# Optimization experiments

Measured on AMD Instinct MI355X. Metric: run time of the kernel, lower is better.

Reference implementation:

```python
import jax, jax.numpy as jnp
import numpy as np

UNITS = 512
IN_DIM = 256


def setup_inputs() -> dict:
    key = jax.random.key(0)
    k1, k2, k3 = jax.random.split(key, 3)
    x = jax.random.normal(k1, (128, 512, IN_DIM), dtype=jnp.float32)
    # glorot_uniform for kernel
    lim = float(np.sqrt(6.0 / (IN_DIM + UNITS)))
    kernel = jax.random.uniform(k2, (IN_DIM, UNITS), minval=-lim, maxval=lim, dtype=jnp.float32)
    # orthogonal init for recurrent kernel
    a = jax.random.normal(k3, (UNITS, UNITS), dtype=jnp.float32)
    q, r = jnp.linalg.qr(a)
    recurrent_kernel = q * jnp.sign(jnp.diag(r))[None, :]
    bias = jnp.zeros((UNITS,), dtype=jnp.float32)
    return {"x": x, "kernel": kernel, "recurrent_kernel": recurrent_kernel, "bias": bias}


def reference(x, kernel, recurrent_kernel, bias):
    # h_t = tanh(x_t @ W_x + b + h_{t-1} @ W_h), return full sequence [B, T, U]
    B = x.shape[0]
    # Precompute input projection for all timesteps in one batched GEMM
    xp = jnp.einsum('btf,fu->btu', x, kernel) + bias  # [B, T, U]

    def step(h, xp_t):
        h_new = jnp.tanh(xp_t + h @ recurrent_kernel)
        return h_new, h_new

    h0 = jnp.zeros((B, UNITS), dtype=x.dtype)
    _, ys = jax.lax.scan(step, h0, jnp.swapaxes(xp, 0, 1))  # ys: [T, B, U]
    return jnp.swapaxes(ys, 0, 1)
```

## Files before the change

kernel.cpp:

```cpp
#include <hip/hip_runtime.h>
#include <math.h>


#define SENT 0xFFFFFFFFu
#define ALF(p)    __hip_atomic_load((p), __ATOMIC_RELAXED, __HIP_MEMORY_SCOPE_AGENT)
#define ASF(p, v) __hip_atomic_store((p), (v), __ATOMIC_RELAXED, __HIP_MEMORY_SCOPE_AGENT)
#define FMA4(A, W, H) { (A).x += (H)*(W).x; (A).y += (H)*(W).y; (A).z += (H)*(W).z; (A).w += (H)*(W).w; }

__global__ __launch_bounds__(256) void xp_gemm_sent(
    const float* __restrict__ x,
    const float* __restrict__ wx,
    const float* __restrict__ bias,
    float* __restrict__ xp,
    float* __restrict__ out)
{
    __shared__ float As[32][68];
    __shared__ float Bs[32][68];

    const int tid = threadIdx.x;
    const int m0 = blockIdx.y * 64;
    const int n0 = blockIdx.x * 64;
    const int tm = tid / 16;
    const int tn = tid % 16;

    {
        const float s = __uint_as_float(SENT);
        const float4 sv = make_float4(s, s, s, s);
        const int r = tid >> 4;
        const int c = (tid & 15) * 4;
        float* op = out + (size_t)m0 * 512 + n0;
        #pragma unroll
        for (int i = 0; i < 4; ++i)
            *(float4*)&op[(size_t)(r + 16 * i) * 512 + c] = sv;
    }

    float acc[4][4] = {};

    for (int k0 = 0; k0 < 256; k0 += 32) {
        {
            const int kk = tid % 32, r0 = tid / 32;
            #pragma unroll
            for (int rr = 0; rr < 8; ++rr)
                As[kk][r0 + rr * 8] = x[(size_t)(m0 + r0 + rr * 8) * 256 + (k0 + kk)];
        }
        {
            const int nn = tid % 64, r0 = tid / 64;
            #pragma unroll
            for (int rr = 0; rr < 8; ++rr)
                Bs[r0 + rr * 4][nn] = wx[(size_t)(k0 + r0 + rr * 4) * 512 + (n0 + nn)];
        }
        __syncthreads();

        #pragma unroll
        for (int kk = 0; kk < 32; ++kk) {
            const float4 a = *(const float4*)&As[kk][tm * 4];
            const float4 b = *(const float4*)&Bs[kk][tn * 4];
            const float av[4] = {a.x, a.y, a.z, a.w};
            const float bv[4] = {b.x, b.y, b.z, b.w};
            #pragma unroll
            for (int i = 0; i < 4; ++i)
                #pragma unroll
                for (int j = 0; j < 4; ++j)
                    acc[i][j] += av[i] * bv[j];
        }
        __syncthreads();
    }

    #pragma unroll
    for (int i = 0; i < 4; ++i)
        #pragma unroll
        for (int j = 0; j < 4; ++j)
            xp[(size_t)(m0 + tm * 4 + i) * 512 + (n0 + tn * 4 + j)] =
                acc[i][j] + bias[n0 + tn * 4 + j];
}

__global__ __launch_bounds__(1024) void rnn_scan9(
    const float* __restrict__ wh,
    const float* __restrict__ xp,
    float* __restrict__ out)
{
    __shared__ float h_lds[2][512];
    __shared__ float red[32][2][128];

    const int tid = threadIdx.x;
    const int us  = blockIdx.x >> 6;
    const int bg  = blockIdx.x & 63;
    const int u0  = us * 128;
    const int g   = tid & 31;
    const int s   = tid >> 5;
    const int kbase = s * 16;
    const size_t seq = 512 * 512;

    const float* wr = &wh[(size_t)kbase * 512 + (u0 + 4 * g)];
    const float4 w0  = *(const float4*)(wr + 0  * 512);
    const float4 w1  = *(const float4*)(wr + 1  * 512);
    const float4 w2  = *(const float4*)(wr + 2  * 512);
    const float4 w3  = *(const float4*)(wr + 3  * 512);
    const float4 w4  = *(const float4*)(wr + 4  * 512);
    const float4 w5  = *(const float4*)(wr + 5  * 512);
    const float4 w6  = *(const float4*)(wr + 6  * 512);
    const float4 w7  = *(const float4*)(wr + 7  * 512);
    const float4 w8  = *(const float4*)(wr + 8  * 512);
    const float4 w9  = *(const float4*)(wr + 9  * 512);
    const float4 w10 = *(const float4*)(wr + 10 * 512);
    const float4 w11 = *(const float4*)(wr + 11 * 512);
    const float4 w12 = *(const float4*)(wr + 12 * 512);
    const float4 w13 = *(const float4*)(wr + 13 * 512);
    const float4 w14 = *(const float4*)(wr + 14 * 512);
    const float4 w15 = *(const float4*)(wr + 15 * 512);

    const int ru = tid & 127;
    const int rb = (tid >> 7) & 1;
    const float* xpp = xp + (size_t)(bg * 2 + rb) * seq + u0 + ru;
    float*       hop = out + (size_t)(bg * 2 + rb) * seq + u0 + ru;

    const int sb   = (tid >= 384) ? 1 : 0;
    const int srem = tid - sb * 384;
    const int shk  = (srem < u0) ? srem : srem + 128;
    const float* pollp = out + (size_t)(bg * 2 + sb) * seq + shk;

    for (int t = 0; t < 512; ++t) {
        float xpv = 0.0f;
        if (tid < 256) xpv = xpp[(size_t)t * 512];

        if (t == 0) {
            ((float*)h_lds)[tid] = 0.0f;
        } else if (tid < 768) {
            const float* p = pollp + (size_t)(t - 1) * 512;
            float v = ALF(p);
            int it = 0;
            while (__float_as_uint(v) == SENT && ++it < (1 << 22)) {
                if (it > 32) __builtin_amdgcn_s_sleep(1);
                v = ALF(p);
            }
            h_lds[sb][shk] = v;
        }
        __syncthreads();

        float4 a0 = make_float4(0.f, 0.f, 0.f, 0.f);
        float4 a1 = make_float4(0.f, 0.f, 0.f, 0.f);
        const float* hb0 = &h_lds[0][kbase];
        const float* hb1 = &h_lds[1][kbase];
        #define STEP4(W0, W1, W2, W3, OFF) { \
            const float4 h0 = *(const float4*)(hb0 + (OFF)); \
            const float4 h1 = *(const float4*)(hb1 + (OFF)); \
            FMA4(a0, W0, h0.x) FMA4(a0, W1, h0.y) FMA4(a0, W2, h0.z) FMA4(a0, W3, h0.w) \
            FMA4(a1, W0, h1.x) FMA4(a1, W1, h1.y) FMA4(a1, W2, h1.z) FMA4(a1, W3, h1.w) }
        STEP4(w0,  w1,  w2,  w3,  0)
        STEP4(w4,  w5,  w6,  w7,  4)
        STEP4(w8,  w9,  w10, w11, 8)
        STEP4(w12, w13, w14, w15, 12)
        #undef STEP4

        *(float4*)&red[s][0][4 * g] = a0;
        *(float4*)&red[s][1][4 * g] = a1;
        __syncthreads();

        if (tid < 256) {
            float r = xpv;
            #pragma unroll
            for (int ss = 0; ss < 32; ++ss) r += red[ss][rb][ru];
            const float hn = tanhf(r);
            ASF(hop + (size_t)t * 512, hn);
            h_lds[rb][u0 + ru] = hn;
        }
    }
}

__global__ __launch_bounds__(256) void xp_gemm_plain(
    const float* __restrict__ x, const float* __restrict__ wx,
    const float* __restrict__ bias, float* __restrict__ xp)
{
    __shared__ float As[32][68];
    __shared__ float Bs[32][68];
    const int tid = threadIdx.x;
    const int m0 = blockIdx.y * 64;
    const int n0 = blockIdx.x * 64;
    const int tm = tid / 16;
    const int tn = tid % 16;
    float acc[4][4] = {};
    for (int k0 = 0; k0 < 256; k0 += 32) {
        {
            const int kk = tid % 32, r0 = tid / 32;
            #pragma unroll
            for (int rr = 0; rr < 8; ++rr)
                As[kk][r0 + rr * 8] = x[(size_t)(m0 + r0 + rr * 8) * 256 + (k0 + kk)];
        }
        {
            const int nn = tid % 64, r0 = tid / 64;
            #pragma unroll
            for (int rr = 0; rr < 8; ++rr)
                Bs[r0 + rr * 4][nn] = wx[(size_t)(k0 + r0 + rr * 4) * 512 + (n0 + nn)];
        }
        __syncthreads();
        #pragma unroll
        for (int kk = 0; kk < 32; ++kk) {
            const float4 a = *(const float4*)&As[kk][tm * 4];
            const float4 b = *(const float4*)&Bs[kk][tn * 4];
            const float av[4] = {a.x, a.y, a.z, a.w};
            const float bv[4] = {b.x, b.y, b.z, b.w};
            #pragma unroll
            for (int i = 0; i < 4; ++i)
                #pragma unroll
                for (int j = 0; j < 4; ++j)
                    acc[i][j] += av[i] * bv[j];
        }
        __syncthreads();
    }
    #pragma unroll
    for (int i = 0; i < 4; ++i)
        #pragma unroll
        for (int j = 0; j < 4; ++j)
            xp[(size_t)(m0 + tm * 4 + i) * 512 + (n0 + tn * 4 + j)] =
                acc[i][j] + bias[n0 + tn * 4 + j];
}

__global__ __launch_bounds__(1024, 4) void rnn_scan2(
    const float* __restrict__ wh, float* __restrict__ out)
{
    __shared__ float h_lds[2][512];
    __shared__ float red[8][2][512];
    const int tid = threadIdx.x;
    const int g = tid & 127;
    const int s = tid >> 7;
    const int b = tid >> 9;
    const int u = tid & 511;
    float* seqb = out + (size_t)(2 * blockIdx.x + b) * 512 * 512;
    h_lds[b][u] = 0.0f;
    __syncthreads();
    const float4* __restrict__ whv = (const float4*)wh;
    const int kbase = s * 64;
    for (int t = 0; t < 512; ++t) {
        const float xpv = seqb[(size_t)t * 512 + u];
        float4 a0 = make_float4(0.f, 0.f, 0.f, 0.f);
        float4 a1 = make_float4(0.f, 0.f, 0.f, 0.f);
        #pragma unroll 4
        for (int kk = 0; kk < 64; kk += 4) {
            const int k = kbase + kk;
            const float4 h0 = *(const float4*)&h_lds[0][k];
            const float4 h1 = *(const float4*)&h_lds[1][k];
            const float4 v0 = whv[(k + 0) * 128 + g];
            const float4 v1 = whv[(k + 1) * 128 + g];
            const float4 v2 = whv[(k + 2) * 128 + g];
            const float4 v3 = whv[(k + 3) * 128 + g];
            FMA4(a0, v0, h0.x) FMA4(a0, v1, h0.y) FMA4(a0, v2, h0.z) FMA4(a0, v3, h0.w)
            FMA4(a1, v0, h1.x) FMA4(a1, v1, h1.y) FMA4(a1, v2, h1.z) FMA4(a1, v3, h1.w)
        }
        *(float4*)&red[s][0][4 * g] = a0;
        *(float4*)&red[s][1][4 * g] = a1;
        __syncthreads();
        float r = xpv;
        #pragma unroll
        for (int ss = 0; ss < 8; ++ss) r += red[ss][b][u];
        const float hn = tanhf(r);
        h_lds[b][u] = hn;
        seqb[(size_t)t * 512 + u] = hn;
        __syncthreads();
    }
}

extern "C" void kernel_launch(void* const* d_in, const int* in_sizes, int n_in,
                              void* d_out, int out_size, void* d_ws, size_t ws_size,
                              hipStream_t stream) {
    const float* x    = (const float*)d_in[0];
    const float* wx   = (const float*)d_in[1];
    const float* wh   = (const float*)d_in[2];
    const float* bias = (const float*)d_in[3];
    float* out = (float*)d_out;

    const size_t xp_bytes = (size_t)128 * 512 * 512 * sizeof(float);
    dim3 g1(512 / 64, 65536 / 64);

    if (d_ws != nullptr && ws_size >= xp_bytes) {
        xp_gemm_sent<<<g1, 256, 0, stream>>>(x, wx, bias, (float*)d_ws, out);
        rnn_scan9<<<256, 1024, 0, stream>>>(wh, (const float*)d_ws, out);
    } else {
        xp_gemm_plain<<<g1, 256, 0, stream>>>(x, wx, bias, out);
        rnn_scan2<<<64, 1024, 0, stream>>>(wh, out);
    }
}
```

Measured before the change: 1.290 ms.

## Overlap own-slice recurrent FMAs with cross-block polling in RNN scan

```diff
diff --git a/kernel.cpp b/kernel.cpp
--- a/kernel.cpp
+++ b/kernel.cpp
@@ -24,8 +24,8 @@
     const int tn = tid % 16;
 
     {
-        const float s = __uint_as_float(SENT);
-        const float4 sv = make_float4(s, s, s, s);
+        const float sv1 = __uint_as_float(SENT);
+        const float4 sv = make_float4(sv1, sv1, sv1, sv1);
         const int r = tid >> 4;
         const int c = (tid & 15) * 4;
         float* op = out + (size_t)m0 * 512 + n0;
@@ -74,7 +74,7 @@
                 acc[i][j] + bias[n0 + tn * 4 + j];
 }
 
-__global__ __launch_bounds__(1024) void rnn_scan9(
+__global__ __launch_bounds__(1024) void rnn_scan10(
     const float* __restrict__ wh,
     const float* __restrict__ xp,
     float* __restrict__ out)
@@ -89,6 +89,7 @@
     const int g   = tid & 31;
     const int s   = tid >> 5;
     const int kbase = s * 16;
+    const bool ownk = ((s >> 3) == us);
     const size_t seq = 512 * 512;
 
     const float* wr = &wh[(size_t)kbase * 512 + (u0 + 4 * g)];
@@ -119,52 +120,72 @@
     const int shk  = (srem < u0) ? srem : srem + 128;
     const float* pollp = out + (size_t)(bg * 2 + sb) * seq + shk;
 
+    #define DO_FMA() { \
+        float4 a0 = make_float4(0.f, 0.f, 0.f, 0.f); \
+        float4 a1 = make_float4(0.f, 0.f, 0.f, 0.f); \
+        const float* hb0 = &h_lds[0][kbase]; \
+        const float* hb1 = &h_lds[1][kbase]; \
+        { const float4 h0 = *(const float4*)(hb0 + 0); \
+          const float4 h1 = *(const float4*)(hb1 + 0); \
+          FMA4(a0, w0, h0.x) FMA4(a0, w1, h0.y) FMA4(a0, w2, h0.z) FMA4(a0, w3, h0.w) \
+          FMA4(a1, w0, h1.x) FMA4(a1, w1, h1.y) FMA4(a1, w2, h1.z) FMA4(a1, w3, h1.w) } \
+        { const float4 h0 = *(const float4*)(hb0 + 4); \
+          const float4 h1 = *(const float4*)(hb1 + 4); \
+          FMA4(a0, w4, h0.x) FMA4(a0, w5, h0.y) FMA4(a0, w6, h0.z) FMA4(a0, w7, h0.w) \
+          FMA4(a1, w4, h1.x) FMA4(a1, w5, h1.y) FMA4(a1, w6, h1.z) FMA4(a1, w7, h1.w) } \
+        { const float4 h0 = *(const float4*)(hb0 + 8); \
+          const float4 h1 = *(const float4*)(hb1 + 8); \
+          FMA4(a0, w8,  h0.x) FMA4(a0, w9,  h0.y) FMA4(a0, w10, h0.z) FMA4(a0, w11, h0.w) \
+          FMA4(a1, w8,  h1.x) FMA4(a1, w9,  h1.y) FMA4(a1, w10, h1.z) FMA4(a1, w11, h1.w) } \
+        { const float4 h0 = *(const float4*)(hb0 + 12); \
+          const float4 h1 = *(const float4*)(hb1 + 12); \
+          FMA4(a0, w12, h0.x) FMA4(a0, w13, h0.y) FMA4(a0, w14, h0.z) FMA4(a0, w15, h0.w) \
+          FMA4(a1, w12, h1.x) FMA4(a1, w13, h1.y) FMA4(a1, w14, h1.z) FMA4(a1, w15, h1.w) } \
+        *(float4*)&red[s][0][4 * g] = a0; \
+        *(float4*)&red[s][1][4 * g] = a1; }
+
     for (int t = 0; t < 512; ++t) {
         float xpv = 0.0f;
         if (tid < 256) xpv = xpp[(size_t)t * 512];
 
+        const float* pp = pollp + (size_t)(t > 0 ? t - 1 : 0) * 512;
+        float pa = 0.f, pb = 0.f;
+        if (t > 0 && tid < 768) {
+            pa = ALF(pp);
+            pb = ALF(pp);
+        }
+
+        if (t > 0 && ownk) DO_FMA();
+
         if (t == 0) {
             ((float*)h_lds)[tid] = 0.0f;
         } else if (tid < 768) {
-            const float* p = pollp + (size_t)(t - 1) * 512;
-            float v = ALF(p);
             int it = 0;
-            while (__float_as_uint(v) == SENT && ++it < (1 << 22)) {
-                if (it > 32) __builtin_amdgcn_s_sleep(1);
-                v = ALF(p);
+            while (__float_as_uint(pa) == SENT && ++it < (1 << 22)) {
+                if (it > 64) __builtin_amdgcn_s_sleep(1);
+                pa = pb;
+                pb = ALF(pp);
             }
-            h_lds[sb][shk] = v;
-        }
-        __syncthreads();
-
-        float4 a0 = make_float4(0.f, 0.f, 0.f, 0.f);
-        float4 a1 = make_float4(0.f, 0.f, 0.f, 0.f);
-        const float* hb0 = &h_lds[0][kbase];
-        const float* hb1 = &h_lds[1][kbase];
-        #define STEP4(W0, W1, W2, W3, OFF) { \
-            const float4 h0 = *(const float4*)(hb0 + (OFF)); \
-            const float4 h1 = *(const float4*)(hb1 + (OFF)); \
-            FMA4(a0, W0, h0.x) FMA4(a0, W1, h0.y) FMA4(a0, W2, h0.z) FMA4(a0, W3, h0.w) \
-            FMA4(a1, W0, h1.x) FMA4(a1, W1, h1.y) FMA4(a1, W2, h1.z) FMA4(a1, W3, h1.w) }
-        STEP4(w0,  w1,  w2,  w3,  0)
-        STEP4(w4,  w5,  w6,  w7,  4)
-        STEP4(w8,  w9,  w10, w11, 8)
-        STEP4(w12, w13, w14, w15, 12)
-        #undef STEP4
-
-        *(float4*)&red[s][0][4 * g] = a0;
-        *(float4*)&red[s][1][4 * g] = a1;
+            h_lds[sb][shk] = pa;
+        }
+        __syncthreads();
+
+        if (t > 0 && !ownk) DO_FMA();
         __syncthreads();
 
         if (tid < 256) {
             float r = xpv;
-            #pragma unroll
-            for (int ss = 0; ss < 32; ++ss) r += red[ss][rb][ru];
+            if (t > 0) {
+                #pragma unroll
+                for (int ss = 0; ss < 32; ++ss) r += red[ss][rb][ru];
+            }
             const float hn = tanhf(r);
             ASF(hop + (size_t)t * 512, hn);
             h_lds[rb][u0 + ru] = hn;
         }
-    }
+        __syncthreads();
+    }
+    #undef DO_FMA
 }
 
 __global__ __launch_bounds__(256) void xp_gemm_plain(
@@ -273,7 +294,7 @@
 
     if (d_ws != nullptr && ws_size >= xp_bytes) {
         xp_gemm_sent<<<g1, 256, 0, stream>>>(x, wx, bias, (float*)d_ws, out);
-        rnn_scan9<<<256, 1024, 0, stream>>>(wh, (const float*)d_ws, out);
+        rnn_scan10<<<256, 1024, 0, stream>>>(wh, (const float*)d_ws, out);
     } else {
         xp_gemm_plain<<<g1, 256, 0, stream>>>(x, wx, bias, out);
         rnn_scan2<<<64, 1024, 0, stream>>>(wh, out);
```

After: 1.361 ms. 1.05x slower.
